# Performance work log

Hardware: AMD Instinct MI355X
Metric: run time of the kernel (lower is better)

The kernel has to match this reference:

```python
import jax, jax.numpy as jnp
import numpy as np

V, E, H = 50257, 256, 128          # vocab, embedding_size, lstm hidden per direction
L, B = 2048, 64                    # seq_len, batch (x is [L, B], seq-first)
SEP, MASK = 50256, 0
SEP_EVERY = 16
N_UTT = L // SEP_EVERY             # utterances per sequence (seps planted regularly)


def setup_inputs() -> dict:
    key = jax.random.key(0)
    ks = jax.random.split(key, 12)
    x = jax.random.randint(ks[0], (L, B), 0, SEP, dtype=jnp.int32)
    # plant sep tokens every SEP_EVERY positions -> each utterance has SEP_EVERY tokens
    x = x.at[SEP_EVERY - 1::SEP_EVERY, :].set(SEP)
    s = 1.0 / np.sqrt(H)
    u = lambda k, sh: jax.random.uniform(k, sh, jnp.float32, -s, s)
    return {
        "x": x,
        "emb": jax.random.normal(ks[1], (V, E), jnp.float32),
        "w_ih_f": u(ks[2], (4 * H, E)), "w_hh_f": u(ks[3], (4 * H, H)),
        "b_ih_f": u(ks[4], (4 * H,)),   "b_hh_f": u(ks[5], (4 * H,)),
        "w_ih_b": u(ks[6], (4 * H, E)), "w_hh_b": u(ks[7], (4 * H, H)),
        "b_ih_b": u(ks[8], (4 * H,)),   "b_hh_b": u(ks[9], (4 * H,)),
        "w_out": u(ks[10], (2, E)),     "b_out": u(ks[11], (2,)),
    }


def _lstm_dir(xu, w_ih, w_hh, b_ih, b_hh, reverse):
    # xu: [T, B, E]; PyTorch LSTM gate order i, f, g, o
    xp = jnp.einsum("tbe,ge->tbg", xu, w_ih) + b_ih + b_hh  # [T, B, 4H]

    def step(carry, xt):
        h, c = carry
        g = xt + h @ w_hh.T
        i, f, gg, o = jnp.split(g, 4, axis=-1)
        c = jax.nn.sigmoid(f) * c + jax.nn.sigmoid(i) * jnp.tanh(gg)
        h = jax.nn.sigmoid(o) * jnp.tanh(c)
        return (h, c), h

    init = (jnp.zeros((xu.shape[1], H), xu.dtype), jnp.zeros((xu.shape[1], H), xu.dtype))
    _, hs = jax.lax.scan(step, init, xp, reverse=reverse)
    return hs  # [T, B, H]


def _forward(x, emb, w_ih_f, w_hh_f, b_ih_f, b_hh_f, w_ih_b, w_hh_b, b_ih_b, b_hh_b, w_out, b_out):
    # --- ragged utterance mean-pool (replaces per-token Python loops) ---
    seps = (x == SEP)
    seg = jnp.cumsum(seps.astype(jnp.int32), axis=0) - seps.astype(jnp.int32)  # [L,B]: utterance id per token (sep ends its utterance)
    gids = (seg * B + jnp.arange(B, dtype=jnp.int32)[None, :]).reshape(L * B)
    tok_emb = emb[x]                                              # [L, B, E]
    sums = jax.ops.segment_sum(tok_emb.reshape(L * B, E), gids, num_segments=N_UTT * B).reshape(N_UTT, B, E)
    cnts = jax.ops.segment_sum(jnp.ones((L * B,), tok_emb.dtype), gids, num_segments=N_UTT * B).reshape(N_UTT, B, 1)
    u = jnp.where(cnts > 0, sums / jnp.maximum(cnts, 1.0), 0.0)   # [N_UTT, B, E] (zeros pad, as original)
    # --- BiLSTM over utterances ---
    h_f = _lstm_dir(u, w_ih_f, w_hh_f, b_ih_f, b_hh_f, reverse=False)
    h_b = _lstm_dir(u, w_ih_b, w_hh_b, b_ih_b, b_hh_b, reverse=True)
    h = jnp.concatenate([h_f, h_b], axis=-1)                      # [N_UTT, B, E]
    logits = jnp.einsum("tbe,oe->tbo", h, w_out) + b_out          # [N_UTT, B, 2]
    policy = jax.nn.softmax(logits, axis=-1)
    # greedy policy (deterministic reference)
    u_mask = jnp.argmax(policy, axis=-1)                          # [N_UTT, B] in {0,1}
    chosen_policy = jnp.take_along_axis(policy, u_mask[..., None], axis=-1)  # [N_UTT, B, 1]
    # expand utterance mask to token mask and mask the input
    token_mask = u_mask.astype(bool)[seg, jnp.arange(B)[None, :]]  # [L, B]
    masked_input = jnp.where(token_mask, x, MASK)
    return logits, policy, chosen_policy, u_mask.astype(bool), masked_input


def reference(x, emb, w_ih_f, w_hh_f, b_ih_f, b_hh_f, w_ih_b, w_hh_b, b_ih_b, b_hh_b, w_out, b_out):
    return _forward(x, emb, w_ih_f, w_hh_f, b_ih_f, b_hh_f, w_ih_b, w_hh_b, b_ih_b, b_hh_b, w_out, b_out)
```

## Files before the change

kernel.cpp:

```cpp
#include <hip/hip_runtime.h>
#include <hip/hip_fp16.h>
#include <math.h>

#define LL   2048
#define BB   64
#define EE   256
#define HH   128
#define GG   512
#define TT   128
#define SEPT 50256

__global__ __launch_bounds__(256) void segscan_k(
    const int* __restrict__ x, int* __restrict__ seg,
    int* __restrict__ cnt, int* __restrict__ start)
{
    int b   = blockIdx.x;
    int tid = threadIdx.x;
    __shared__ int tsum[256];
    __shared__ int ucnt[TT];
    __shared__ int ustart[TT];

    int flags[8];
    int local = 0;
#pragma unroll
    for (int i = 0; i < 8; i++) {
        int t = tid * 8 + i;
        flags[i] = (x[t * BB + b] == SEPT) ? 1 : 0;
        local += flags[i];
    }
    tsum[tid] = local;
    __syncthreads();
    int val = local;
    for (int off = 1; off < 256; off <<= 1) {
        int other = (tid >= off) ? tsum[tid - off] : 0;
        __syncthreads();
        val += other;
        tsum[tid] = val;
        __syncthreads();
    }
    int excl = val - local;

    if (tid < TT) ucnt[tid] = 0;
    __syncthreads();
    int run = excl;
#pragma unroll
    for (int i = 0; i < 8; i++) {
        int t = tid * 8 + i;
        int s = run;
        seg[t * BB + b] = s;
        run += flags[i];
        if (s < TT) atomicAdd(&ucnt[s], 1);
    }
    __syncthreads();
    if (tid == 0) {
        int acc = 0;
        for (int u = 0; u < TT; u++) { ustart[u] = acc; acc += ucnt[u]; }
    }
    __syncthreads();
    if (tid < TT) {
        cnt[tid * BB + b]   = ucnt[tid];
        start[tid * BB + b] = ustart[tid];
    }
}

__global__ __launch_bounds__(256) void pool_k(
    const int* __restrict__ x, const float* __restrict__ emb,
    const int* __restrict__ cnt, const int* __restrict__ start,
    float* __restrict__ up)
{
    int wid  = threadIdx.x >> 6;
    int lane = threadIdx.x & 63;
    int bid  = blockIdx.x * 4 + wid;
    int b    = bid & 63;
    int c    = cnt[bid];
    int st   = start[bid];

    float4 acc = {0.f, 0.f, 0.f, 0.f};
    int tok = (c > 0) ? x[st * BB + b] : 0;
    for (int j = 0; j < c; j++) {
        int tok_n = (j + 1 < c) ? x[(st + j + 1) * BB + b] : 0;
        float4 v = ((const float4*)(emb + (size_t)tok * EE))[lane];
        acc.x += v.x; acc.y += v.y; acc.z += v.z; acc.w += v.w;
        tok = tok_n;
    }
    float inv = (c > 0) ? 1.f / (float)c : 0.f;
    float4 r = {acc.x * inv, acc.y * inv, acc.z * inv, acc.w * inv};
    ((float4*)(up + (size_t)bid * EE))[lane] = r;
}

__global__ __launch_bounds__(256) void xp_gemm_k(
    const float* __restrict__ A,
    const float* __restrict__ wf, const float* __restrict__ wb,
    const float* __restrict__ bihf, const float* __restrict__ bhhf,
    const float* __restrict__ bihb, const float* __restrict__ bhhb,
    float* __restrict__ C)
{
    __shared__ float As[32][128];
    __shared__ float Bs[32][128];
    int tid  = threadIdx.x;
    int row0 = blockIdx.x * 128;
    int col0 = blockIdx.y * 128;
    int tx = tid & 15, ty = tid >> 4;
    float acc[8][8] = {};

    for (int k0 = 0; k0 < EE; k0 += 32) {
#pragma unroll
        for (int i = 0; i < 4; i++) {
            int idx = tid + i * 256;
            int m   = idx >> 3;
            int k4  = idx & 7;
            float4 av = *(const float4*)(A + (size_t)(row0 + m) * EE + k0 + k4 * 4);
            As[k4 * 4 + 0][m] = av.x; As[k4 * 4 + 1][m] = av.y;
            As[k4 * 4 + 2][m] = av.z; As[k4 * 4 + 3][m] = av.w;
        }
#pragma unroll
        for (int i = 0; i < 4; i++) {
            int idx = tid + i * 256;
            int n   = idx >> 3;
            int k4  = idx & 7;
            int gc  = col0 + n;
            const float* wsrc = (gc < GG) ? (wf + (size_t)gc * EE)
                                          : (wb + (size_t)(gc - GG) * EE);
            float4 bv = *(const float4*)(wsrc + k0 + k4 * 4);
            Bs[k4 * 4 + 0][n] = bv.x; Bs[k4 * 4 + 1][n] = bv.y;
            Bs[k4 * 4 + 2][n] = bv.z; Bs[k4 * 4 + 3][n] = bv.w;
        }
        __syncthreads();
#pragma unroll
        for (int k = 0; k < 32; k++) {
            float a8[8], b8[8];
            *(float4*)&a8[0] = *(const float4*)&As[k][ty * 8 + 0];
            *(float4*)&a8[4] = *(const float4*)&As[k][ty * 8 + 4];
            *(float4*)&b8[0] = *(const float4*)&Bs[k][tx * 8 + 0];
            *(float4*)&b8[4] = *(const float4*)&Bs[k][tx * 8 + 4];
#pragma unroll
            for (int i = 0; i < 8; i++)
#pragma unroll
                for (int j = 0; j < 8; j++)
                    acc[i][j] += a8[i] * b8[j];
        }
        __syncthreads();
    }

    float bias[8];
#pragma unroll
    for (int j = 0; j < 8; j++) {
        int gc = col0 + tx * 8 + j;
        bias[j] = (gc < GG) ? (bihf[gc] + bhhf[gc])
                            : (bihb[gc - GG] + bhhb[gc - GG]);
    }
#pragma unroll
    for (int i = 0; i < 8; i++) {
        int r = row0 + ty * 8 + i;
        float4 v0 = {acc[i][0] + bias[0], acc[i][1] + bias[1],
                     acc[i][2] + bias[2], acc[i][3] + bias[3]};
        float4 v1 = {acc[i][4] + bias[4], acc[i][5] + bias[5],
                     acc[i][6] + bias[6], acc[i][7] + bias[7]};
        *(float4*)(C + (size_t)r * 1024 + col0 + tx * 8 + 0) = v0;
        *(float4*)(C + (size_t)r * 1024 + col0 + tx * 8 + 4) = v1;
    }
}

__device__ __forceinline__ float sigm_f(float x) {
    return 1.f / (1.f + __expf(-x));
}
__device__ __forceinline__ float tanh_f(float x) {
    return 1.f - 2.f / (__expf(2.f * x) + 1.f);
}

__global__ __launch_bounds__(256) void cvt_k(
    const float* __restrict__ wf, const float* __restrict__ wb,
    __half* __restrict__ o)
{
    int i = blockIdx.x * 256 + threadIdx.x;
    int e   = i & 7;
    int g   = (i >> 3) & 511;
    int q   = (i >> 12) & 15;
    int dir = i >> 16;
    const float* src = dir ? wb : wf;
    o[i] = __float2half(src[(size_t)g * HH + q * 8 + e]);
}

typedef _Float16 h2v __attribute__((ext_vector_type(2)));
__device__ __forceinline__ float dot2h(unsigned wbits, unsigned hbits, float c) {
    return __builtin_amdgcn_fdot2(__builtin_bit_cast(h2v, wbits),
                                  __builtin_bit_cast(h2v, hbits), c, false);
}

__global__ __launch_bounds__(512, 2) void lstm_rec_k(
    const float* __restrict__ xp,
    const __half* __restrict__ w16,
    float* __restrict__ hout)
{
    int bid = blockIdx.x;
    int dir = bid >> 6;
    int b   = bid & 63;
    int tid = threadIdx.x;
    int g   = tid;
    int sect = g >> 7;
    const uint4* wp = (const uint4*)(w16 + (size_t)dir * (16 * GG * 8));

    __shared__ uint4 wlds[8 * GG];
    __shared__ __align__(16) __half h16_lds[HH];
    __shared__ float act[GG];

#pragma unroll
    for (int t = 0; t < 8; t++) {
        int idx = tid + t * 512;
        wlds[idx] = wp[idx];
    }

    uint4 q8[8];
#pragma unroll
    for (int q = 0; q < 8; q++)
        q8[q] = wp[(q + 8) * GG + g];
#pragma unroll
    for (int q = 0; q < 8; q++) {
        asm volatile("" : "+v"(q8[q].x), "+v"(q8[q].y),
                          "+v"(q8[q].z), "+v"(q8[q].w));
    }

    float c = 0.f;
    if (tid < HH) h16_lds[tid] = __float2half(0.f);
    __syncthreads();

    const uint4* h16v = (const uint4*)h16_lds;

    int t0   = dir ? (TT - 1) : 0;
    float xg = xp[(size_t)(t0 * BB + b) * 1024 + dir * GG + g];

    for (int s = 0; s < TT; s++) {
        float acc = xg;
#pragma unroll
        for (int q = 0; q < 8; q++) {
            uint4 w = wlds[q * GG + g];
            uint4 hv = h16v[q];
            acc = dot2h(w.x, hv.x, acc);
            acc = dot2h(w.y, hv.y, acc);
            acc = dot2h(w.z, hv.z, acc);
            acc = dot2h(w.w, hv.w, acc);
        }
#pragma unroll
        for (int q = 0; q < 8; q++) {
            uint4 w = q8[q];
            uint4 hv = h16v[q + 8];
            acc = dot2h(w.x, hv.x, acc);
            acc = dot2h(w.y, hv.y, acc);
            acc = dot2h(w.z, hv.z, acc);
            acc = dot2h(w.w, hv.w, acc);
        }

        act[g] = (sect == 2) ? tanh_f(acc) : sigm_f(acc);

        float xg_next = xg;
        if (s < TT - 1) {
            int tn = dir ? (TT - 2 - s) : (s + 1);
            xg_next = xp[(size_t)(tn * BB + b) * 1024 + dir * GG + g];
        }
        __syncthreads();

        if (tid < HH) {
            float si = act[tid], sf = act[HH + tid];
            float tg = act[2 * HH + tid], so = act[3 * HH + tid];
            c = sf * c + si * tg;
            float h = so * tanh_f(c);
            h16_lds[tid] = __float2half(h);
            int t = dir ? (TT - 1 - s) : s;
            hout[((size_t)(dir * TT + t) * BB + b) * HH + tid] = h;
        }
        xg = xg_next;
        __syncthreads();
    }
}

__global__ __launch_bounds__(256) void head_k(
    const float* __restrict__ hbuf,
    const float* __restrict__ wout, const float* __restrict__ bout,
    float* __restrict__ out)
{
    int wid  = threadIdx.x >> 6;
    int lane = threadIdx.x & 63;
    int row  = blockIdx.x * 4 + wid;
    int t = row >> 6, b = row & 63;
    const float* hf = hbuf + ((size_t)(t)      * BB + b) * HH;
    const float* hb = hbuf + ((size_t)(TT + t) * BB + b) * HH;

    float l0 = 0.f, l1 = 0.f, v;
    v = hf[lane];      l0 += v * wout[lane];           l1 += v * wout[256 + lane];
    v = hf[lane + 64]; l0 += v * wout[64 + lane];      l1 += v * wout[320 + lane];
    v = hb[lane];      l0 += v * wout[128 + lane];     l1 += v * wout[384 + lane];
    v = hb[lane + 64]; l0 += v * wout[192 + lane];     l1 += v * wout[448 + lane];
#pragma unroll
    for (int off = 32; off > 0; off >>= 1) {
        l0 += __shfl_down(l0, off);
        l1 += __shfl_down(l1, off);
    }
    if (lane == 0) {
        l0 += bout[0]; l1 += bout[1];
        float m  = fmaxf(l0, l1);
        float e0 = __expf(l0 - m), e1 = __expf(l1 - m);
        float inv = 1.f / (e0 + e1);
        float p0 = e0 * inv, p1 = e1 * inv;
        int amax = (l1 > l0) ? 1 : 0;
        out[(size_t)row * 2 + 0] = l0;
        out[(size_t)row * 2 + 1] = l1;
        out[16384 + (size_t)row * 2 + 0] = p0;
        out[16384 + (size_t)row * 2 + 1] = p1;
        out[32768 + row] = amax ? p1 : p0;
        out[40960 + row] = (float)amax;
    }
}

__global__ __launch_bounds__(256) void mask_k(
    const int* __restrict__ x, const int* __restrict__ seg,
    const float* __restrict__ umask, float* __restrict__ out4)
{
    int idx = blockIdx.x * 256 + threadIdx.x;
    int b = idx & 63;
    int s = seg[idx];
    if (s > TT - 1) s = TT - 1;
    if (s < 0) s = 0;
    float keep = umask[s * BB + b];
    out4[idx] = (keep != 0.f) ? (float)x[idx] : 0.f;
}

extern "C" void kernel_launch(void* const* d_in, const int* in_sizes, int n_in,
                              void* d_out, int out_size, void* d_ws, size_t ws_size,
                              hipStream_t stream)
{
    const int*   x    = (const int*)  d_in[0];
    const float* emb  = (const float*)d_in[1];
    const float* wihf = (const float*)d_in[2];
    const float* whhf = (const float*)d_in[3];
    const float* bihf = (const float*)d_in[4];
    const float* bhhf = (const float*)d_in[5];
    const float* wihb = (const float*)d_in[6];
    const float* whhb = (const float*)d_in[7];
    const float* bihb = (const float*)d_in[8];
    const float* bhhb = (const float*)d_in[9];
    const float* wout = (const float*)d_in[10];
    const float* bout = (const float*)d_in[11];
    float* out = (float*)d_out;
    char*  ws  = (char*)d_ws;

    int*   seg   = (int*)  (ws + 0);
    int*   cnt   = (int*)  (ws + 524288);
    int*   start = (int*)  (ws + 557056);
    float* up    = (float*)(ws + 589824);
    float* xp    = (float*)(ws + 8978432);
    float* hbuf  = (float*)(ws + 42532864);
    __half* wh16 = (__half*)up;

    segscan_k<<<64, 256, 0, stream>>>(x, seg, cnt, start);
    pool_k<<<2048, 256, 0, stream>>>(x, emb, cnt, start, up);
    xp_gemm_k<<<dim3(64, 8), 256, 0, stream>>>(up, wihf, wihb, bihf, bhhf, bihb, bhhb, xp);
    cvt_k<<<512, 256, 0, stream>>>(whhf, whhb, wh16);
    lstm_rec_k<<<128, 512, 0, stream>>>(xp, wh16, hbuf);
    head_k<<<2048, 256, 0, stream>>>(hbuf, wout, bout, out);
    mask_k<<<512, 256, 0, stream>>>(x, seg, out + 40960, out + 49152);
}
```

Baseline: 287.4 us.

## Use split-fp16 MFMA for input projection GEMM instead of FP32 FMA

Rewrites the xp_gemm kernel so each fp32 operand is split into high and low fp16 parts in shared memory. The product is accumulated with three 16x16x32 f16 MFMA instructions (hi*hi, lo*hi, hi*lo) to stay close to fp32 accuracy. This targets the FP32 scalar FMA cost of the projection GEMM. It adds conversion work, four shared tiles and scalar (non-vectorized) output stores, and loses the lo*lo term.

```diff
diff --git a/kernel.cpp b/kernel.cpp
--- a/kernel.cpp
+++ b/kernel.cpp
@@ -88,6 +88,9 @@
     ((float4*)(up + (size_t)bid * EE))[lane] = r;
 }
 
+typedef _Float16 f16x8 __attribute__((ext_vector_type(8)));
+typedef float f32x4 __attribute__((ext_vector_type(4)));
+
 __global__ __launch_bounds__(256) void xp_gemm_k(
     const float* __restrict__ A,
     const float* __restrict__ wf, const float* __restrict__ wb,
@@ -95,69 +98,94 @@
     const float* __restrict__ bihb, const float* __restrict__ bhhb,
     float* __restrict__ C)
 {
-    __shared__ float As[32][128];
-    __shared__ float Bs[32][128];
-    int tid  = threadIdx.x;
-    int row0 = blockIdx.x * 128;
-    int col0 = blockIdx.y * 128;
-    int tx = tid & 15, ty = tid >> 4;
-    float acc[8][8] = {};
+    __shared__ _Float16 Ahi[128 * 40];
+    __shared__ _Float16 Alo[128 * 40];
+    __shared__ _Float16 Bhi[128 * 40];
+    __shared__ _Float16 Blo[128 * 40];
+    int tid = threadIdx.x;
+    int m0 = blockIdx.x * 128;
+    int n0 = blockIdx.y * 128;
+    int wave = tid >> 6, l = tid & 63;
+    int wm = wave >> 1, wn = wave & 1;
+    int lr = l & 15, lk = l >> 4;
+    int srow = tid >> 1, shalf = tid & 1;
+
+    f32x4 acc[4][4] = {};
 
     for (int k0 = 0; k0 < EE; k0 += 32) {
+        const float* ga = A + (size_t)(m0 + srow) * EE + k0 + shalf * 16;
+        int gc = n0 + srow;
+        const float* gw = ((gc < GG) ? (wf + (size_t)gc * EE)
+                                     : (wb + (size_t)(gc - GG) * EE))
+                          + k0 + shalf * 16;
+        float av[16], bv[16];
 #pragma unroll
         for (int i = 0; i < 4; i++) {
-            int idx = tid + i * 256;
-            int m   = idx >> 3;
-            int k4  = idx & 7;
-            float4 av = *(const float4*)(A + (size_t)(row0 + m) * EE + k0 + k4 * 4);
-            As[k4 * 4 + 0][m] = av.x; As[k4 * 4 + 1][m] = av.y;
-            As[k4 * 4 + 2][m] = av.z; As[k4 * 4 + 3][m] = av.w;
-        }
-#pragma unroll
-        for (int i = 0; i < 4; i++) {
-            int idx = tid + i * 256;
-            int n   = idx >> 3;
-            int k4  = idx & 7;
-            int gc  = col0 + n;
-            const float* wsrc = (gc < GG) ? (wf + (size_t)gc * EE)
-                                          : (wb + (size_t)(gc - GG) * EE);
-            float4 bv = *(const float4*)(wsrc + k0 + k4 * 4);
-            Bs[k4 * 4 + 0][n] = bv.x; Bs[k4 * 4 + 1][n] = bv.y;
-            Bs[k4 * 4 + 2][n] = bv.z; Bs[k4 * 4 + 3][n] = bv.w;
-        }
-        __syncthreads();
-#pragma unroll
-        for (int k = 0; k < 32; k++) {
-            float a8[8], b8[8];
-            *(float4*)&a8[0] = *(const float4*)&As[k][ty * 8 + 0];
-            *(float4*)&a8[4] = *(const float4*)&As[k][ty * 8 + 4];
-            *(float4*)&b8[0] = *(const float4*)&Bs[k][tx * 8 + 0];
-            *(float4*)&b8[4] = *(const float4*)&Bs[k][tx * 8 + 4];
-#pragma unroll
-            for (int i = 0; i < 8; i++)
-#pragma unroll
-                for (int j = 0; j < 8; j++)
-                    acc[i][j] += a8[i] * b8[j];
-        }
-        __syncthreads();
-    }
-
-    float bias[8];
-#pragma unroll
-    for (int j = 0; j < 8; j++) {
-        int gc = col0 + tx * 8 + j;
-        bias[j] = (gc < GG) ? (bihf[gc] + bhhf[gc])
-                            : (bihb[gc - GG] + bhhb[gc - GG]);
-    }
-#pragma unroll
-    for (int i = 0; i < 8; i++) {
-        int r = row0 + ty * 8 + i;
-        float4 v0 = {acc[i][0] + bias[0], acc[i][1] + bias[1],
-                     acc[i][2] + bias[2], acc[i][3] + bias[3]};
-        float4 v1 = {acc[i][4] + bias[4], acc[i][5] + bias[5],
-                     acc[i][6] + bias[6], acc[i][7] + bias[7]};
-        *(float4*)(C + (size_t)r * 1024 + col0 + tx * 8 + 0) = v0;
-        *(float4*)(C + (size_t)r * 1024 + col0 + tx * 8 + 4) = v1;
+            *(float4*)&av[i * 4] = *(const float4*)(ga + i * 4);
+            *(float4*)&bv[i * 4] = *(const float4*)(gw + i * 4);
+        }
+        _Float16 ah[16], al[16], bh[16], bl[16];
+#pragma unroll
+        for (int e = 0; e < 16; e++) {
+            _Float16 h = (_Float16)av[e];
+            ah[e] = h;  al[e] = (_Float16)(av[e] - (float)h);
+            _Float16 hb = (_Float16)bv[e];
+            bh[e] = hb; bl[e] = (_Float16)(bv[e] - (float)hb);
+        }
+        int base = srow * 40 + shalf * 16;
+        *(uint4*)&Ahi[base]     = *(uint4*)&ah[0];
+        *(uint4*)&Ahi[base + 8] = *(uint4*)&ah[8];
+        *(uint4*)&Alo[base]     = *(uint4*)&al[0];
+        *(uint4*)&Alo[base + 8] = *(uint4*)&al[8];
+        *(uint4*)&Bhi[base]     = *(uint4*)&bh[0];
+        *(uint4*)&Bhi[base + 8] = *(uint4*)&bh[8];
+        *(uint4*)&Blo[base]     = *(uint4*)&bl[0];
+        *(uint4*)&Blo[base + 8] = *(uint4*)&bl[8];
+        __syncthreads();
+
+        f16x8 bhif[4], blof[4];
+#pragma unroll
+        for (int nf = 0; nf < 4; nf++) {
+            int boff = (wn * 64 + nf * 16 + lr) * 40 + lk * 8;
+            bhif[nf] = *(const f16x8*)&Bhi[boff];
+            blof[nf] = *(const f16x8*)&Blo[boff];
+        }
+#pragma unroll
+        for (int mf = 0; mf < 4; mf++) {
+            int aoff = (wm * 64 + mf * 16 + lr) * 40 + lk * 8;
+            f16x8 ahif = *(const f16x8*)&Ahi[aoff];
+            f16x8 alof = *(const f16x8*)&Alo[aoff];
+#pragma unroll
+            for (int nf = 0; nf < 4; nf++) {
+                acc[mf][nf] = __builtin_amdgcn_mfma_f32_16x16x32_f16(
+                    ahif, bhif[nf], acc[mf][nf], 0, 0, 0);
+                acc[mf][nf] = __builtin_amdgcn_mfma_f32_16x16x32_f16(
+                    alof, bhif[nf], acc[mf][nf], 0, 0, 0);
+                acc[mf][nf] = __builtin_amdgcn_mfma_f32_16x16x32_f16(
+                    ahif, blof[nf], acc[mf][nf], 0, 0, 0);
+            }
+        }
+        __syncthreads();
+    }
+
+    float bias[4];
+#pragma unroll
+    for (int nf = 0; nf < 4; nf++) {
+        int gc = n0 + wn * 64 + nf * 16 + lr;
+        bias[nf] = (gc < GG) ? (bihf[gc] + bhhf[gc])
+                             : (bihb[gc - GG] + bhhb[gc - GG]);
+    }
+#pragma unroll
+    for (int mf = 0; mf < 4; mf++) {
+#pragma unroll
+        for (int nf = 0; nf < 4; nf++) {
+            int n = n0 + wn * 64 + nf * 16 + lr;
+#pragma unroll
+            for (int r = 0; r < 4; r++) {
+                int m = m0 + wm * 64 + mf * 16 + lk * 4 + r;
+                C[(size_t)m * 1024 + n] = acc[mf][nf][r] + bias[nf];
+            }
+        }
     }
 }
 
```

Result: faster. 246.4 us (-14.2%).
